# Kernel optimization log

Hardware: AMD Instinct MI355X
Metric: run time of the kernel (lower is better)

The kernel has to match this reference:

```python
import jax, jax.numpy as jnp
import numpy as np

N = 30000       # num atoms (all examples concatenated)
E = 480000      # total num edges (avg degree 16)
H = 128         # hidden_channels
R = 50          # num_rbf
NB = 3          # num interaction blocks
NEX = 64        # num examples (molecules)
NTYPES = 100    # atom type vocabulary
CUT = 10.0      # cutoff_upper


def setup_inputs() -> dict:
    key = jax.random.key(0)
    ks = jax.random.split(key, 20)
    s = 0.05
    inp = {
        "pos": jax.random.uniform(ks[0], (N, 3), dtype=jnp.float32) * 10.0,
        "atom_types": jax.random.randint(ks[1], (N,), 0, NTYPES),
        "edge_index": jax.random.randint(ks[2], (2, E), 0, N),
        "batch": jnp.sort(jax.random.randint(ks[3], (N,), 0, NEX)),
        # learned parameters
        "embedding": jax.random.normal(ks[4], (NTYPES, H), dtype=jnp.float32) * s,
        "filt_w1": jax.random.normal(ks[5], (NB, R, H), dtype=jnp.float32) * s,
        "filt_b1": jnp.zeros((NB, H), jnp.float32),
        "filt_w2": jax.random.normal(ks[6], (NB, H, H), dtype=jnp.float32) * s,
        "filt_b2": jnp.zeros((NB, H), jnp.float32),
        "lin1_w": jax.random.normal(ks[7], (NB, H, H), dtype=jnp.float32) * s,  # no bias
        "lin2_w": jax.random.normal(ks[8], (NB, H, H), dtype=jnp.float32) * s,
        "lin2_b": jnp.zeros((NB, H), jnp.float32),
        "blk_w": jax.random.normal(ks[9], (NB, H, H), dtype=jnp.float32) * s,
        "blk_b": jnp.zeros((NB, H), jnp.float32),
        "out_w1": jax.random.normal(ks[10], (H, H // 2), dtype=jnp.float32) * s,
        "out_b1": jnp.zeros((H // 2,), jnp.float32),
        "out_w2": jax.random.normal(ks[11], (H // 2, 1), dtype=jnp.float32) * s,
        "out_b2": jnp.zeros((1,), jnp.float32),
    }
    return inp


def reference(pos, atom_types, edge_index, batch, embedding,
              filt_w1, filt_b1, filt_w2, filt_b2,
              lin1_w, lin2_w, lin2_b, blk_w, blk_b,
              out_w1, out_b1, out_w2, out_b2):
    src, dst = edge_index[0], edge_index[1]
    # pairwise distances along edges
    diff = pos[src] - pos[dst]                        # [E,3]
    d = jnp.sqrt(jnp.sum(diff * diff, axis=-1) + 1e-12)  # [E]
    # Gaussian RBF expansion (PyG GaussianSmearing)
    offset = jnp.linspace(0.0, CUT, R, dtype=jnp.float32)
    coeff = -0.5 / (offset[1] - offset[0]) ** 2
    rbf = jnp.exp(coeff * (d[:, None] - offset) ** 2)  # [E,R]
    # cosine cutoff envelope
    C = 0.5 * (jnp.cos(d * jnp.pi / CUT) + 1.0) * (d < CUT)  # [E]

    x = embedding[atom_types]                         # [N,H]
    for b in range(NB):
        # filter network: Linear -> Tanh -> Linear, modulated by cutoff
        W = jnp.tanh(rbf @ filt_w1[b] + filt_b1[b]) @ filt_w2[b] + filt_b2[b]
        W = W * C[:, None]                            # [E,H]
        # cfconv: lin1 (no bias), gather-multiply-scatter, lin2
        h = x @ lin1_w[b]                             # [N,H]
        msg = h[src] * W                              # [E,H]
        agg = jax.ops.segment_sum(msg, dst, num_segments=N)  # [N,H]
        h = agg @ lin2_w[b] + lin2_b[b]
        # interaction block: activation + linear, residual update
        x = x + (jnp.tanh(h) @ blk_w[b] + blk_b[b])
    # output network: per-atom energy then scatter-sum per molecule
    e = jnp.tanh(x @ out_w1 + out_b1) @ out_w2 + out_b2     # [N,1]
    energy = jax.ops.segment_sum(e, batch, num_segments=NEX)  # [NEX,1]
    return energy.reshape(-1)
```

## Files before the change

kernel.cpp:

```cpp
#include <hip/hip_runtime.h>

typedef unsigned short ushort_t;
typedef _Float16 half8 __attribute__((ext_vector_type(8)));
typedef float f32x4 __attribute__((ext_vector_type(4)));

constexpr int NN  = 30000;
constexpr int EE  = 480000;
constexpr int NEXM = 64;
constexpr int ATB = 16;
constexpr int NSB = (NN + 255) / 256;
constexpr int NBINS = 2048;
constexpr int TROWS = 2064;

#define MFMA16(a,b,c) __builtin_amdgcn_mfma_f32_16x16x32_f16((a),(b),(c),0,0,0)
#define LDS_ADD(p,v) __hip_atomic_fetch_add((p),(v),__ATOMIC_RELAXED,__HIP_MEMORY_SCOPE_WORKGROUP)
#define LGKM_WAIT asm volatile("s_waitcnt lgkmcnt(0)" ::: "memory")

__device__ __forceinline__ float fast_tanh(float x){
  float e2 = __builtin_amdgcn_exp2f(x * 2.885390081777927f);
  return 1.f - 2.f * __builtin_amdgcn_rcpf(e2 + 1.f);
}
__device__ __forceinline__ ushort_t f2h(float v){
  union { _Float16 h; ushort_t s; } cv; cv.h = (_Float16)v; return cv.s;
}

__global__ __launch_bounds__(256) void prep_weights(
  const float* __restrict__ fw1, const float* __restrict__ fb1,
  const float* __restrict__ fw2, const float* __restrict__ l1w,
  const float* __restrict__ l2w, const float* __restrict__ bw,
  const float* __restrict__ ow1, ushort_t* __restrict__ frags)
{
  int u = blockIdx.x*256 + threadIdx.x;
  float val;
  if (u < 24576){
    int b = u >> 13; int v = u & 8191;
    int j = v & 7, lane = (v>>3)&63, fid = v>>9;
    int mt = fid>>1, ks = fid&1;
    int f1 = mt*16 + (lane&15);
    int k  = ks*32 + ((lane>>4)&3)*8 + j;
    val = (k < 50) ? fw1[(b*50 + k)*128 + f1] : (k == 50 ? fb1[b*128 + f1] : 0.f);
  } else if (u < 73728){
    int v = u - 24576; int b = v >> 14; int v2 = v & 16383;
    int j = v2&7, lane = (v2>>3)&63, fid = v2>>9;
    int mt = fid>>2, ks = fid&3;
    int n = mt*16 + (lane&15);
    int k = ks*32 + ((lane>>4)&3)*8 + j;
    val = fw2[b*16384 + k*128 + n];
  } else if (u < 221184){
    int v = u - 73728; int g = v / 49152; int v1 = v - g*49152;
    int b = v1 >> 14; int v2 = v1 & 16383;
    int j = v2&7, lane=(v2>>3)&63, fid=v2>>9;
    int mt = fid>>2, ks = fid&3;
    int n = mt*16 + (lane&15);
    int k = ks*32 + ((lane>>4)&3)*8 + j;
    const float* W = (g==0? l2w : (g==1? bw : l1w));
    val = W[b*16384 + k*128 + n];
  } else {
    int v2 = u - 221184;
    int j = v2&7, lane=(v2>>3)&63, fid=v2>>9;
    int mt = fid>>2, ks = fid&3;
    int n = mt*16 + (lane&15);
    int k = ks*32 + ((lane>>4)&3)*8 + j;
    val = ow1[k*64 + n];
  }
  frags[u] = f2h(val);
}

__global__ __launch_bounds__(256) void count_k(
  const int* __restrict__ ei, int* __restrict__ cnt)
{
  int e = blockIdx.x*256 + threadIdx.x;
  atomicAdd(cnt + ei[EE + e], 1);
}

__global__ __launch_bounds__(256) void scan1(
  const int* __restrict__ cnt, int* __restrict__ seg, int* __restrict__ bsum)
{
  __shared__ int ws[4];
  int i = blockIdx.x*256 + threadIdx.x;
  int lane = threadIdx.x & 63, w = threadIdx.x >> 6;
  int v = (i < NN) ? cnt[i] : 0;
  int s = v;
  #pragma unroll
  for (int o=1;o<64;o<<=1){ int t = __shfl_up(s,o,64); if (lane>=o) s += t; }
  if (lane == 63) ws[w] = s;
  __syncthreads();
  int add = 0;
  #pragma unroll
  for (int j=0;j<3;j++) if (w > j) add += ws[j];
  s += add;
  if (i < NN) seg[i] = s - v;
  if (threadIdx.x == 255) bsum[blockIdx.x] = s;
}

__global__ __launch_bounds__(128) void scan2(int* __restrict__ bsum)
{
  __shared__ int w0tot;
  int tid = threadIdx.x, lane = tid & 63, w = tid >> 6;
  int v = (tid < NSB) ? bsum[tid] : 0;
  int s = v;
  #pragma unroll
  for (int o=1;o<64;o<<=1){ int t = __shfl_up(s,o,64); if (lane>=o) s += t; }
  if (w == 0 && lane == 63) w0tot = s;
  __syncthreads();
  if (w == 1) s += w0tot;
  if (tid < NSB) bsum[tid] = s - v;
}

__global__ __launch_bounds__(256) void scan3(
  int* __restrict__ seg, const int* __restrict__ bsum)
{
  int i = blockIdx.x*256 + threadIdx.x;
  if (i < NN) seg[i] += bsum[blockIdx.x];
}

__global__ __launch_bounds__(256) void scatter_meta(
  const float* __restrict__ pos, const int* __restrict__ ei,
  int* __restrict__ off, uint2* __restrict__ meta2)
{
  int e = blockIdx.x*256 + threadIdx.x;
  int s = ei[e], d = ei[EE + e];
  float dx = pos[s*3+0]-pos[d*3+0];
  float dy = pos[s*3+1]-pos[d*3+1];
  float dz = pos[s*3+2]-pos[d*3+2];
  float dist = sqrtf(dx*dx+dy*dy+dz*dz + 1e-12f);
  float t = fminf(dist, 10.f) * ((float)NBINS / 10.f);
  int p = atomicAdd(off + d, 1);
  uint2 m;
  m.x = __float_as_uint(t);
  m.y = (unsigned)s;
  meta2[p] = m;
}

__global__ __launch_bounds__(256) void build_table(
  const ushort_t* __restrict__ w1a, const ushort_t* __restrict__ w2a,
  const float* __restrict__ fb2, ushort_t* __restrict__ tab)
{
  __shared__ ushort_t st[4*2112];
  const int wave = threadIdx.x>>6, lane = threadIdx.x&63;
  const int quad = lane>>4, n15 = lane&15;
  const int b = blockIdx.x / 33, tg = blockIdx.x % 33;
  const int tile = tg*4 + wave;
  if (tile >= TROWS/16) return;
  const half8* w1v = (const half8*)(w1a + b*8192);
  const half8* w2v = (const half8*)(w2a + b*16384);
  ushort_t* tw = st + wave*2112;
  half8 a1[16];
  #pragma unroll
  for (int i=0;i<16;i++) a1[i] = w1v[i*64 + lane];
  f32x4 b2v[8];
  #pragma unroll
  for (int mt=0;mt<8;mt++) b2v[mt] = *(const f32x4*)(fb2 + b*128 + mt*16 + quad*4);
  const f32x4 zero4 = {0.f,0.f,0.f,0.f};
  const float dd = 10.f/49.f;
  const float coefl2 = (-0.5f/(dd*dd)) * 1.4426950408889634f;
  const float dbin = 10.f/(float)NBINS;

  float de = (float)(tile*16 + n15) * dbin;
  float Cv = (de < 10.f) ? 0.5f*(cosf(de*0.31415926535897931f)+1.f) : 0.f;
  half8 rb0, rb1;
  #pragma unroll
  for (int j=0;j<8;j++){
    int k0 = quad*8 + j;
    float t0 = de - (float)k0*dd;
    rb0[j] = (_Float16)__builtin_amdgcn_exp2f(coefl2*t0*t0);
    int k1 = 32 + quad*8 + j;
    float v1;
    if (k1 < 50){ float t1 = de - (float)k1*dd; v1 = __builtin_amdgcn_exp2f(coefl2*t1*t1); }
    else v1 = (k1 == 50) ? 1.f : 0.f;
    rb1[j] = (_Float16)v1;
  }
  f32x4 acc1[8];
  #pragma unroll
  for (int mt=0;mt<8;mt++){
    acc1[mt] = MFMA16(a1[mt*2],   rb0, zero4);
    acc1[mt] = MFMA16(a1[mt*2+1], rb1, acc1[mt]);
  }
  #pragma unroll
  for (int mt=0;mt<8;mt++){
    union { ushort_t s[4]; uint2 v; } pk;
    #pragma unroll
    for (int r=0;r<4;r++) pk.s[r] = f2h(fast_tanh(acc1[mt][r]));
    *(uint2*)(tw + n15*132 + mt*16 + quad*4) = pk.v;
  }
  LGKM_WAIT;
  f32x4 acc2[8];
  #pragma unroll
  for (int mt=0;mt<8;mt++) acc2[mt] = zero4;
  #pragma unroll
  for (int ks=0;ks<4;ks++){
    const ushort_t* ra = tw + n15*132 + ks*32 + quad*8;
    union { uint2 v[2]; half8 h16; } cc;
    cc.v[0] = *(const uint2*)(ra);
    cc.v[1] = *(const uint2*)(ra + 4);
    half8 tb = cc.h16;
    #pragma unroll
    for (int mt=0;mt<8;mt++) acc2[mt] = MFMA16(w2v[(mt*4+ks)*64 + lane], tb, acc2[mt]);
  }
  LGKM_WAIT;
  #pragma unroll
  for (int mt=0;mt<8;mt++){
    f32x4 v = acc2[mt] + b2v[mt];
    union { ushort_t s[4]; uint2 q; } pk;
    #pragma unroll
    for (int r=0;r<4;r++) pk.s[r] = f2h(v[r] * Cv);
    *(uint2*)(tw + n15*132 + mt*16 + quad*4) = pk.q;
  }
  LGKM_WAIT;
  ushort_t* dstb = tab + ((size_t)b*TROWS + tile*16)*128;
  #pragma unroll
  for (int it=0;it<4;it++){
    int off = it*512 + lane*8;
    uint4 v = *(const uint4*)(tw + (off>>7)*132 + (off&127));
    *(uint4*)(dstb + (size_t)(off>>7)*128 + (off&127)) = v;
  }
}

__global__ __launch_bounds__(256) void embed_h0(
  const int* __restrict__ atype, const float* __restrict__ emb,
  const ushort_t* __restrict__ l1T, float* __restrict__ x, ushort_t* __restrict__ h)
{
  __shared__ float xbuf[4*2112];
  const int wave = threadIdx.x>>6, lane = threadIdx.x&63;
  const int quad = lane>>4, n15 = lane&15;
  float* xw = xbuf + wave*2112;
  ushort_t* sw = (ushort_t*)xw;
  const half8* wv = (const half8*)l1T;
  const f32x4 zero4 = {0.f,0.f,0.f,0.f};
  const int ntiles = NN/16;
  const int stride = gridDim.x*4;
  for (int tile = blockIdx.x*4 + wave; tile < ntiles; tile += stride){
    int a0 = tile*16;
    int typ = atype[a0 + n15];
    const f32x4* av = (const f32x4*)(emb + (size_t)typ*128);
    half8 bg[4]; f32x4 xl[4], xh[4];
    #pragma unroll
    for (int ks=0;ks<4;ks++){
      f32x4 lo = av[ks*8 + quad*2];
      f32x4 hi = av[ks*8 + quad*2 + 1];
      xl[ks] = lo; xh[ks] = hi;
      half8 bh;
      #pragma unroll
      for (int i=0;i<4;i++){ bh[i]=(_Float16)lo[i]; bh[4+i]=(_Float16)hi[i]; }
      bg[ks] = bh;
    }
    f32x4 acc[8];
    #pragma unroll
    for (int mt=0;mt<8;mt++) acc[mt] = zero4;
    #pragma unroll
    for (int ks=0;ks<4;ks++){
      #pragma unroll
      for (int mt=0;mt<8;mt++) acc[mt] = MFMA16(wv[(mt*4+ks)*64 + lane], bg[ks], acc[mt]);
    }
    #pragma unroll
    for (int ks=0;ks<4;ks++){
      *(f32x4*)(xw + n15*132 + ks*32 + quad*8)     = xl[ks];
      *(f32x4*)(xw + n15*132 + ks*32 + quad*8 + 4) = xh[ks];
    }
    LGKM_WAIT;
    {
      float* gx = x + (size_t)a0*128;
      #pragma unroll
      for (int it=0;it<8;it++){
        int off = it*256 + lane*4;
        f32x4 v = *(const f32x4*)(xw + (off>>7)*132 + (off&127));
        *(f32x4*)(gx + off) = v;
      }
    }
    LGKM_WAIT;
    #pragma unroll
    for (int mt=0;mt<8;mt++){
      union { ushort_t s[4]; uint2 v; } pk;
      #pragma unroll
      for (int r=0;r<4;r++) pk.s[r] = f2h(acc[mt][r]);
      *(uint2*)(sw + n15*132 + mt*16 + quad*4) = pk.v;
    }
    LGKM_WAIT;
    {
      ushort_t* gh = h + (size_t)a0*128;
      #pragma unroll
      for (int it=0;it<4;it++){
        int off = it*512 + lane*8;
        uint4 v = *(const uint4*)(sw + (off>>7)*132 + (off&127));
        *(uint4*)(gh + off) = v;
      }
    }
    LGKM_WAIT;
  }
}

__global__ __launch_bounds__(256,6) void mega_pass(
  const uint2* __restrict__ meta2, const ushort_t* __restrict__ hin,
  ushort_t* __restrict__ hout, const ushort_t* __restrict__ tab,
  const ushort_t* __restrict__ l2T, const ushort_t* __restrict__ bkT,
  const ushort_t* __restrict__ l1Tn,
  const float* __restrict__ l2b, const float* __restrict__ bb,
  const int* __restrict__ segend, float* __restrict__ x, int do_h)
{
  __shared__ ushort_t nt[2112];
  const int wave = threadIdx.x>>6, lane = threadIdx.x&63;
  const int quad = lane>>4, n15 = lane&15;
  const int base = blockIdx.x*ATB;
  const f32x4 zero4 = {0.f,0.f,0.f,0.f};

  const int cg = threadIdx.x >> 4, ctf = threadIdx.x & 15;
  const int ca = base + cg;
  const int clo = (ca==0) ? 0 : segend[ca-1];
  const int chi = segend[ca];
  float acc[8];
  #pragma unroll
  for (int j=0;j<8;j++) acc[j] = 0.f;

  if (clo < chi){
    uint2 me = *(const uint2*)(meta2 + clo);
    float t = __uint_as_float(me.x);
    int i0 = (int)t;
    float fr = t - (float)i0;
    const half8* tp = (const half8*)(tab + (size_t)i0*128) + ctf;
    half8 w0 = tp[0];
    half8 w1 = tp[16];
    half8 hv = *(const half8*)(hin + (size_t)me.y*128 + ctf*8);
    int e = clo;
    while (true){
      int en = e + 1;
      bool more = en < chi;
      half8 w0n = w0, w1n = w1, hvn = hv; float frn = fr;
      if (more){
        uint2 m2 = *(const uint2*)(meta2 + en);
        float t2 = __uint_as_float(m2.x);
        int i2 = (int)t2;
        frn = t2 - (float)i2;
        const half8* tpn = (const half8*)(tab + (size_t)i2*128) + ctf;
        w0n = tpn[0];
        w1n = tpn[16];
        hvn = *(const half8*)(hin + (size_t)m2.y*128 + ctf*8);
      }
      #pragma unroll
      for (int j=0;j<8;j++){
        float wl = (float)w0[j] + fr * ((float)w1[j] - (float)w0[j]);
        acc[j] += wl * (float)hv[j];
      }
      if (!more) break;
      w0 = w0n; w1 = w1n; hv = hvn; fr = frn; e = en;
    }
  }

  {
    union { ushort_t s[8]; uint4 q; } pk;
    #pragma unroll
    for (int j=0;j<8;j++) pk.s[j] = f2h(acc[j]);
    *(uint4*)(nt + cg*132 + ctf*8) = pk.q;
  }
  __syncthreads();

  {
    half8 bg[4];
    #pragma unroll
    for (int ks=0;ks<4;ks++){
      const ushort_t* ra = nt + n15*132 + ks*32 + quad*8;
      union { uint2 v[2]; half8 h16; } cc;
      cc.v[0] = *(const uint2*)(ra);
      cc.v[1] = *(const uint2*)(ra + 4);
      bg[ks] = cc.h16;
    }
    __syncthreads();
    const half8* wAv = (const half8*)l2T;
    f32x4 accA[2];
    #pragma unroll
    for (int i=0;i<2;i++) accA[i] = zero4;
    #pragma unroll
    for (int ks=0;ks<4;ks++){
      #pragma unroll
      for (int i=0;i<2;i++)
        accA[i] = MFMA16(wAv[((wave*2+i)*4+ks)*64 + lane], bg[ks], accA[i]);
    }
    #pragma unroll
    for (int i=0;i<2;i++){
      int mt = wave*2 + i;
      f32x4 bv = *(const f32x4*)(l2b + mt*16 + quad*4);
      union { ushort_t s[4]; uint2 v; } pk;
      #pragma unroll
      for (int r=0;r<4;r++) pk.s[r] = f2h(fast_tanh(accA[i][r] + bv[r]));
      *(uint2*)(nt + n15*132 + mt*16 + quad*4) = pk.v;
    }
    __syncthreads();
    half8 bg2[4];
    #pragma unroll
    for (int ks=0;ks<4;ks++){
      const ushort_t* ra = nt + n15*132 + ks*32 + quad*8;
      union { uint2 v[2]; half8 h16; } cc;
      cc.v[0] = *(const uint2*)(ra);
      cc.v[1] = *(const uint2*)(ra + 4);
      bg2[ks] = cc.h16;
    }
    __syncthreads();
    const half8* wBv = (const half8*)bkT;
    f32x4 accB[2];
    #pragma unroll
    for (int i=0;i<2;i++) accB[i] = zero4;
    #pragma unroll
    for (int ks=0;ks<4;ks++){
      #pragma unroll
      for (int i=0;i<2;i++)
        accB[i] = MFMA16(wBv[((wave*2+i)*4+ks)*64 + lane], bg2[ks], accB[i]);
    }
    f32x4 xn[2];
    float* xp = x + (size_t)(base + n15)*128;
    #pragma unroll
    for (int i=0;i<2;i++){
      int mt = wave*2 + i;
      f32x4 bv = *(const f32x4*)(bb + mt*16 + quad*4);
      f32x4 xv = *(const f32x4*)(xp + mt*16 + quad*4);
      xn[i] = xv + accB[i] + bv;
      *(f32x4*)(xp + mt*16 + quad*4) = xn[i];
    }
    if (do_h){
      #pragma unroll
      for (int i=0;i<2;i++){
        int mt = wave*2 + i;
        union { ushort_t s[4]; uint2 v; } pk;
        #pragma unroll
        for (int r=0;r<4;r++) pk.s[r] = f2h(xn[i][r]);
        *(uint2*)(nt + n15*132 + mt*16 + quad*4) = pk.v;
      }
      __syncthreads();
      half8 bg3[4];
      #pragma unroll
      for (int ks=0;ks<4;ks++){
        const ushort_t* ra = nt + n15*132 + ks*32 + quad*8;
        union { uint2 v[2]; half8 h16; } cc;
        cc.v[0] = *(const uint2*)(ra);
        cc.v[1] = *(const uint2*)(ra + 4);
        bg3[ks] = cc.h16;
      }
      const half8* wCv = (const half8*)l1Tn;
      f32x4 accC[2];
      #pragma unroll
      for (int i=0;i<2;i++) accC[i] = zero4;
      #pragma unroll
      for (int ks=0;ks<4;ks++){
        #pragma unroll
        for (int i=0;i<2;i++)
          accC[i] = MFMA16(wCv[((wave*2+i)*4+ks)*64 + lane], bg3[ks], accC[i]);
      }
      ushort_t* hp = hout + (size_t)(base + n15)*128;
      #pragma unroll
      for (int i=0;i<2;i++){
        int mt = wave*2 + i;
        union { ushort_t s[4]; uint2 v; } pk;
        #pragma unroll
        for (int r=0;r<4;r++) pk.s[r] = f2h(accC[i][r]);
        *(uint2*)(hp + mt*16 + quad*4) = pk.v;
      }
    }
  }
}

__global__ __launch_bounds__(256) void out_head(
  const float* __restrict__ x, const ushort_t* __restrict__ o1T,
  const float* __restrict__ ob1, const float* __restrict__ ow2,
  const float* __restrict__ ob2, const int* __restrict__ batch,
  float* __restrict__ out)
{
  __shared__ float part[NEXM];
  const int tid = threadIdx.x;
  if (tid < NEXM) part[tid] = 0.f;
  __syncthreads();
  const int wave = tid>>6, lane = tid&63;
  const int quad = lane>>4, n15 = lane&15;
  const half8* wv = (const half8*)o1T;
  const f32x4 zero4 = {0.f,0.f,0.f,0.f};
  f32x4 ow2v[4], ob1v[4];
  #pragma unroll
  for (int mt=0;mt<4;mt++){
    ow2v[mt] = *(const f32x4*)(ow2 + mt*16 + quad*4);
    ob1v[mt] = *(const f32x4*)(ob1 + mt*16 + quad*4);
  }
  const float ob2v = ob2[0];
  const int ntiles = NN/16;
  const int stride = gridDim.x*4;
  for (int tile = blockIdx.x*4 + wave; tile < ntiles; tile += stride){
    int a0 = tile*16;
    half8 bg[4];
    const f32x4* av = (const f32x4*)(x + (size_t)(a0 + n15)*128);
    #pragma unroll
    for (int ks=0;ks<4;ks++){
      f32x4 lo = av[ks*8 + quad*2];
      f32x4 hi = av[ks*8 + quad*2 + 1];
      half8 bh;
      #pragma unroll
      for (int i=0;i<4;i++){ bh[i]=(_Float16)lo[i]; bh[4+i]=(_Float16)hi[i]; }
      bg[ks] = bh;
    }
    f32x4 acc[4];
    #pragma unroll
    for (int mt=0;mt<4;mt++) acc[mt] = zero4;
    #pragma unroll
    for (int ks=0;ks<4;ks++){
      #pragma unroll
      for (int mt=0;mt<4;mt++) acc[mt] = MFMA16(wv[(mt*4+ks)*64 + lane], bg[ks], acc[mt]);
    }
    float e = 0.f;
    #pragma unroll
    for (int mt=0;mt<4;mt++){
      f32x4 v = acc[mt] + ob1v[mt];
      #pragma unroll
      for (int r=0;r<4;r++) e += fast_tanh(v[r]) * ow2v[mt][r];
    }
    e += __shfl_xor(e, 16, 64);
    e += __shfl_xor(e, 32, 64);
    if (quad == 0){
      int a = a0 + n15;
      LDS_ADD(&part[batch[a]], e + ob2v);
    }
  }
  __syncthreads();
  if (tid < NEXM)
    __hip_atomic_fetch_add(out + tid, part[tid], __ATOMIC_RELAXED, __HIP_MEMORY_SCOPE_AGENT);
}

extern "C" void kernel_launch(void* const* d_in, const int* in_sizes, int n_in,
                              void* d_out, int out_size, void* d_ws, size_t ws_size,
                              hipStream_t stream)
{
  const float* pos  = (const float*)d_in[0];
  const int*   atyp = (const int*)  d_in[1];
  const int*   ei   = (const int*)  d_in[2];
  const int*   bat  = (const int*)  d_in[3];
  const float* emb  = (const float*)d_in[4];
  const float* fw1  = (const float*)d_in[5];
  const float* fb1  = (const float*)d_in[6];
  const float* fw2  = (const float*)d_in[7];
  const float* fb2  = (const float*)d_in[8];
  const float* l1w  = (const float*)d_in[9];
  const float* l2w  = (const float*)d_in[10];
  const float* l2b  = (const float*)d_in[11];
  const float* bw   = (const float*)d_in[12];
  const float* bb   = (const float*)d_in[13];
  const float* ow1  = (const float*)d_in[14];
  const float* ob1  = (const float*)d_in[15];
  const float* ow2  = (const float*)d_in[16];
  const float* ob2  = (const float*)d_in[17];
  float* out = (float*)d_out;

  char* p = (char*)d_ws;
  uint2*    meta2 = (uint2*)p;   p += (size_t)EE*8;
  ushort_t* hA   = (ushort_t*)p; p += (size_t)NN*128*2;
  ushort_t* hB   = (ushort_t*)p; p += (size_t)NN*128*2;
  float*    x    = (float*)p;    p += (size_t)NN*128*4;
  ushort_t* frags = (ushort_t*)p; p += 229376*2;
  int*      segend = (int*)p;    p += (size_t)NN*4;
  int*      bsum  = (int*)p;     p += 512;
  ushort_t* tab  = (ushort_t*)p; p += (size_t)3*TROWS*128*2;

  int* cnt = (int*)x;

  ushort_t* w1T = frags;
  ushort_t* w2T = frags + 24576;
  ushort_t* l2T = frags + 73728;
  ushort_t* bkT = frags + 122880;
  ushort_t* l1T = frags + 172032;
  ushort_t* o1T = frags + 221184;

  hipMemsetAsync(d_out, 0, NEXM*sizeof(float), stream);
  hipMemsetAsync(cnt, 0, NN*sizeof(int), stream);
  prep_weights<<<896,256,0,stream>>>(fw1,fb1,fw2,l1w,l2w,bw,ow1,frags);
  build_table<<<99,256,0,stream>>>(w1T, w2T, fb2, tab);
  count_k<<<EE/256,256,0,stream>>>(ei, cnt);
  scan1<<<NSB,256,0,stream>>>(cnt, segend, bsum);
  scan2<<<1,128,0,stream>>>(bsum);
  scan3<<<NSB,256,0,stream>>>(segend, bsum);
  scatter_meta<<<EE/256,256,0,stream>>>(pos, ei, segend, meta2);
  embed_h0<<<512,256,0,stream>>>(atyp, emb, l1T, x, hA);

  for (int b=0;b<3;b++){
    const ushort_t* hin = (b & 1) ? hB : hA;
    ushort_t*       hoB = (b & 1) ? hA : hB;
    int do_h = (b < 2) ? 1 : 0;
    mega_pass<<<NN/ATB,256,0,stream>>>(meta2, hin, hoB,
                                       tab + (size_t)b*TROWS*128,
                                       l2T + b*16384, bkT + b*16384,
                                       l1T + ((b<2)?(b+1):0)*16384,
                                       l2b + b*128, bb + b*128,
                                       segend, x, do_h);
  }
  out_head<<<256,256,0,stream>>>(x, o1T, ob1, ow2, ob2, bat, out);
}
```

Before: 305.1 us.

## Interleave adjacent filter table rows and process two edges per loop iteration

```diff
diff --git a/kernel.cpp b/kernel.cpp
--- a/kernel.cpp
+++ b/kernel.cpp
@@ -134,7 +134,7 @@
 
 __global__ __launch_bounds__(256) void build_table(
   const ushort_t* __restrict__ w1a, const ushort_t* __restrict__ w2a,
-  const float* __restrict__ fb2, ushort_t* __restrict__ tab)
+  const float* __restrict__ fb2, ushort_t* __restrict__ tabP)
 {
   __shared__ ushort_t st[4*2112];
   const int wave = threadIdx.x>>6, lane = threadIdx.x&63;
@@ -207,12 +207,16 @@
     *(uint2*)(tw + n15*132 + mt*16 + quad*4) = pk.q;
   }
   LGKM_WAIT;
-  ushort_t* dstb = tab + ((size_t)b*TROWS + tile*16)*128;
+  ushort_t* dstb = tabP + (size_t)b*TROWS*256;
   #pragma unroll
   for (int it=0;it<4;it++){
     int off = it*512 + lane*8;
-    uint4 v = *(const uint4*)(tw + (off>>7)*132 + (off&127));
-    *(uint4*)(dstb + (size_t)(off>>7)*128 + (off&127)) = v;
+    int rl = off>>7, c = (off&127)>>3;
+    uint4 v = *(const uint4*)(tw + rl*132 + (off&127));
+    int R = tile*16 + rl;
+    *(uint4*)(dstb + (size_t)R*256 + c*16) = v;
+    if (R > 0)
+      *(uint4*)(dstb + (size_t)(R-1)*256 + c*16 + 8) = v;
   }
 }
 
@@ -291,7 +295,7 @@
 
 __global__ __launch_bounds__(256,6) void mega_pass(
   const uint2* __restrict__ meta2, const ushort_t* __restrict__ hin,
-  ushort_t* __restrict__ hout, const ushort_t* __restrict__ tab,
+  ushort_t* __restrict__ hout, const ushort_t* __restrict__ tabP,
   const ushort_t* __restrict__ l2T, const ushort_t* __restrict__ bkT,
   const ushort_t* __restrict__ l1Tn,
   const float* __restrict__ l2b, const float* __restrict__ bb,
@@ -312,36 +316,67 @@
   for (int j=0;j<8;j++) acc[j] = 0.f;
 
   if (clo < chi){
-    uint2 me = *(const uint2*)(meta2 + clo);
-    float t = __uint_as_float(me.x);
-    int i0 = (int)t;
-    float fr = t - (float)i0;
-    const half8* tp = (const half8*)(tab + (size_t)i0*128) + ctf;
-    half8 w0 = tp[0];
-    half8 w1 = tp[16];
-    half8 hv = *(const half8*)(hin + (size_t)me.y*128 + ctf*8);
+    const ushort_t* tbc  = tabP + ctf*16;
+    const ushort_t* hinc = hin + ctf*8;
+    uint2 m0 = meta2[clo];
+    uint2 m1 = (clo+1 < chi) ? meta2[clo+1] : m0;
+    float tA0 = __uint_as_float(m0.x);
+    int   iA0 = (int)tA0;  float fA0 = tA0 - (float)iA0;
+    const ushort_t* pA0 = tbc + (size_t)iA0*256;
+    half8 w0A0 = *(const half8*)pA0;
+    half8 w1A0 = *(const half8*)(pA0 + 8);
+    half8 hvA0 = *(const half8*)(hinc + (size_t)m0.y*128);
+    float tA1 = __uint_as_float(m1.x);
+    int   iA1 = (int)tA1;  float fA1 = tA1 - (float)iA1;
+    const ushort_t* pA1 = tbc + (size_t)iA1*256;
+    half8 w0A1 = *(const half8*)pA1;
+    half8 w1A1 = *(const half8*)(pA1 + 8);
+    half8 hvA1 = *(const half8*)(hinc + (size_t)m1.y*128);
     int e = clo;
-    while (true){
-      int en = e + 1;
-      bool more = en < chi;
-      half8 w0n = w0, w1n = w1, hvn = hv; float frn = fr;
-      if (more){
-        uint2 m2 = *(const uint2*)(meta2 + en);
-        float t2 = __uint_as_float(m2.x);
-        int i2 = (int)t2;
-        frn = t2 - (float)i2;
-        const half8* tpn = (const half8*)(tab + (size_t)i2*128) + ctf;
-        w0n = tpn[0];
-        w1n = tpn[16];
-        hvn = *(const half8*)(hin + (size_t)m2.y*128 + ctf*8);
+    uint2 n0, n1;
+    if (e+2 < chi){
+      n0 = meta2[e+2];
+      n1 = (e+3 < chi) ? meta2[e+3] : n0;
+    }
+    for (;;){
+      const bool hasNext = (e+2 < chi);
+      float fB0=fA0, fB1=fA1;
+      half8 w0B0=w0A0, w1B0=w1A0, hvB0=hvA0;
+      half8 w0B1=w0A1, w1B1=w1A1, hvB1=hvA1;
+      if (hasNext){
+        float tB0 = __uint_as_float(n0.x);
+        int iB0 = (int)tB0;  fB0 = tB0 - (float)iB0;
+        const ushort_t* pB0 = tbc + (size_t)iB0*256;
+        w0B0 = *(const half8*)pB0;
+        w1B0 = *(const half8*)(pB0 + 8);
+        hvB0 = *(const half8*)(hinc + (size_t)n0.y*128);
+        float tB1 = __uint_as_float(n1.x);
+        int iB1 = (int)tB1;  fB1 = tB1 - (float)iB1;
+        const ushort_t* pB1 = tbc + (size_t)iB1*256;
+        w0B1 = *(const half8*)pB1;
+        w1B1 = *(const half8*)(pB1 + 8);
+        hvB1 = *(const half8*)(hinc + (size_t)n1.y*128);
+        if (e+4 < chi){
+          n0 = meta2[e+4];
+          n1 = (e+5 < chi) ? meta2[e+5] : n0;
+        }
       }
       #pragma unroll
       for (int j=0;j<8;j++){
-        float wl = (float)w0[j] + fr * ((float)w1[j] - (float)w0[j]);
-        acc[j] += wl * (float)hv[j];
-      }
-      if (!more) break;
-      w0 = w0n; w1 = w1n; hv = hvn; fr = frn; e = en;
+        float wl = (float)w0A0[j] + fA0 * ((float)w1A0[j] - (float)w0A0[j]);
+        acc[j] += wl * (float)hvA0[j];
+      }
+      if (e+1 < chi){
+        #pragma unroll
+        for (int j=0;j<8;j++){
+          float wl = (float)w0A1[j] + fA1 * ((float)w1A1[j] - (float)w0A1[j]);
+          acc[j] += wl * (float)hvA1[j];
+        }
+      }
+      if (!hasNext) break;
+      fA0=fB0; w0A0=w0B0; w1A0=w1B0; hvA0=hvB0;
+      fA1=fB1; w0A1=w0B1; w1A1=w1B1; hvA1=hvB1;
+      e += 2;
     }
   }
 
@@ -551,7 +586,7 @@
   ushort_t* frags = (ushort_t*)p; p += 229376*2;
   int*      segend = (int*)p;    p += (size_t)NN*4;
   int*      bsum  = (int*)p;     p += 512;
-  ushort_t* tab  = (ushort_t*)p; p += (size_t)3*TROWS*128*2;
+  ushort_t* tabP = (ushort_t*)p; p += (size_t)3*TROWS*256*2;
 
   int* cnt = (int*)x;
 
@@ -565,7 +600,7 @@
   hipMemsetAsync(d_out, 0, NEXM*sizeof(float), stream);
   hipMemsetAsync(cnt, 0, NN*sizeof(int), stream);
   prep_weights<<<896,256,0,stream>>>(fw1,fb1,fw2,l1w,l2w,bw,ow1,frags);
-  build_table<<<99,256,0,stream>>>(w1T, w2T, fb2, tab);
+  build_table<<<99,256,0,stream>>>(w1T, w2T, fb2, tabP);
   count_k<<<EE/256,256,0,stream>>>(ei, cnt);
   scan1<<<NSB,256,0,stream>>>(cnt, segend, bsum);
   scan2<<<1,128,0,stream>>>(bsum);
@@ -578,7 +613,7 @@
     ushort_t*       hoB = (b & 1) ? hA : hB;
     int do_h = (b < 2) ? 1 : 0;
     mega_pass<<<NN/ATB,256,0,stream>>>(meta2, hin, hoB,
-                                       tab + (size_t)b*TROWS*128,
+                                       tabP + (size_t)b*TROWS*256,
                                        l2T + b*16384, bkT + b*16384,
                                        l1T + ((b<2)?(b+1):0)*16384,
                                        l2b + b*128, bb + b*128,
```

After: 335.3 us. 1.1x slower.

## Split each atom's edge aggregation across four lane groups with shuffle reduction

Applied to the files above, without the earlier changes.

```diff
diff --git a/kernel.cpp b/kernel.cpp
--- a/kernel.cpp
+++ b/kernel.cpp
@@ -207,7 +207,7 @@
     *(uint2*)(tw + n15*132 + mt*16 + quad*4) = pk.q;
   }
   LGKM_WAIT;
-  ushort_t* dstb = tab + ((size_t)b*TROWS + tile*16)*128;
+  ushort_t* dstb = tab + ((size_t)tile*16)*128 + (size_t)b*TROWS*128;
   #pragma unroll
   for (int it=0;it<4;it++){
     int off = it*512 + lane*8;
@@ -302,54 +302,70 @@
   const int quad = lane>>4, n15 = lane&15;
   const int base = blockIdx.x*ATB;
   const f32x4 zero4 = {0.f,0.f,0.f,0.f};
-
-  const int cg = threadIdx.x >> 4, ctf = threadIdx.x & 15;
-  const int ca = base + cg;
-  const int clo = (ca==0) ? 0 : segend[ca-1];
-  const int chi = segend[ca];
-  float acc[8];
-  #pragma unroll
-  for (int j=0;j<8;j++) acc[j] = 0.f;
-
-  if (clo < chi){
-    uint2 me = *(const uint2*)(meta2 + clo);
-    float t = __uint_as_float(me.x);
-    int i0 = (int)t;
-    float fr = t - (float)i0;
-    const half8* tp = (const half8*)(tab + (size_t)i0*128) + ctf;
-    half8 w0 = tp[0];
-    half8 w1 = tp[16];
-    half8 hv = *(const half8*)(hin + (size_t)me.y*128 + ctf*8);
-    int e = clo;
-    while (true){
-      int en = e + 1;
-      bool more = en < chi;
-      half8 w0n = w0, w1n = w1, hvn = hv; float frn = fr;
-      if (more){
-        uint2 m2 = *(const uint2*)(meta2 + en);
-        float t2 = __uint_as_float(m2.x);
-        int i2 = (int)t2;
-        frn = t2 - (float)i2;
-        const half8* tpn = (const half8*)(tab + (size_t)i2*128) + ctf;
-        w0n = tpn[0];
-        w1n = tpn[16];
-        hvn = *(const half8*)(hin + (size_t)m2.y*128 + ctf*8);
+  const int sub = lane>>4, ctf = lane&15;
+
+  #pragma unroll 1
+  for (int q=0; q<4; ++q){
+    const int cg = wave*4 + q;
+    const int ca = base + cg;
+    const int clo = (ca==0) ? 0 : segend[ca-1];
+    const int chi = segend[ca];
+    float acc[8];
+    #pragma unroll
+    for (int j=0;j<8;j++) acc[j] = 0.f;
+
+    if (clo < chi){
+      const int elast = chi - 1;
+      int e0 = clo + sub;
+      uint2 mcur = meta2[(e0 < chi) ? e0 : elast];
+      int e1 = clo + 4 + sub;
+      uint2 mnxt = meta2[(e1 < chi) ? e1 : elast];
+      float t0 = __uint_as_float(mcur.x);
+      int i0 = (int)t0; float fr = t0 - (float)i0;
+      const half8* tp = (const half8*)(tab + (size_t)i0*128) + ctf;
+      half8 w0 = tp[0];
+      half8 w1 = tp[16];
+      half8 hv = *(const half8*)(hin + (size_t)mcur.y*128 + ctf*8);
+      bool val = (e0 < chi);
+
+      for (int eb = clo; ; ){
+        int ebn = eb + 4;
+        bool more = ebn < chi;
+        half8 w0n=w0, w1n=w1, hvn=hv; float frn=fr; bool valn=val;
+        if (more){
+          float tn = __uint_as_float(mnxt.x);
+          int in_ = (int)tn; frn = tn - (float)in_;
+          const half8* tpn = (const half8*)(tab + (size_t)in_*128) + ctf;
+          w0n = tpn[0];
+          w1n = tpn[16];
+          hvn = *(const half8*)(hin + (size_t)mnxt.y*128 + ctf*8);
+          valn = (ebn + sub < chi);
+          int e2 = ebn + 4 + sub;
+          mnxt = meta2[(e2 < chi) ? e2 : elast];
+        }
+        if (val){
+          #pragma unroll
+          for (int j=0;j<8;j++){
+            float wl = (float)w0[j] + fr * ((float)w1[j] - (float)w0[j]);
+            acc[j] += wl * (float)hv[j];
+          }
+        }
+        if (!more) break;
+        w0=w0n; w1=w1n; hv=hvn; fr=frn; val=valn; eb=ebn;
       }
-      #pragma unroll
-      for (int j=0;j<8;j++){
-        float wl = (float)w0[j] + fr * ((float)w1[j] - (float)w0[j]);
-        acc[j] += wl * (float)hv[j];
-      }
-      if (!more) break;
-      w0 = w0n; w1 = w1n; hv = hvn; fr = frn; e = en;
-    }
-  }
-
-  {
-    union { ushort_t s[8]; uint4 q; } pk;
-    #pragma unroll
-    for (int j=0;j<8;j++) pk.s[j] = f2h(acc[j]);
-    *(uint4*)(nt + cg*132 + ctf*8) = pk.q;
+    }
+
+    #pragma unroll
+    for (int j=0;j<8;j++){
+      acc[j] += __shfl_xor(acc[j], 16, 64);
+      acc[j] += __shfl_xor(acc[j], 32, 64);
+    }
+    if (sub == 0){
+      union { ushort_t s[8]; uint4 qv; } pk;
+      #pragma unroll
+      for (int j=0;j<8;j++) pk.s[j] = f2h(acc[j]);
+      *(uint4*)(nt + cg*132 + ctf*8) = pk.qv;
+    }
   }
   __syncthreads();
 
```

New measurement: 307.9 us. About the same (+0.9%).

## Pack edge metadata, pair table rows, balance edge gather per wave, fuse output head

Applied to the files above, without the earlier changes.

```diff
diff --git a/kernel.cpp b/kernel.cpp
--- a/kernel.cpp
+++ b/kernel.cpp
@@ -116,7 +116,7 @@
 
 __global__ __launch_bounds__(256) void scatter_meta(
   const float* __restrict__ pos, const int* __restrict__ ei,
-  int* __restrict__ off, uint2* __restrict__ meta2)
+  int* __restrict__ off, unsigned* __restrict__ meta1)
 {
   int e = blockIdx.x*256 + threadIdx.x;
   int s = ei[e], d = ei[EE + e];
@@ -125,11 +125,10 @@
   float dz = pos[s*3+2]-pos[d*3+2];
   float dist = sqrtf(dx*dx+dy*dy+dz*dz + 1e-12f);
   float t = fminf(dist, 10.f) * ((float)NBINS / 10.f);
+  int bin = (int)t;
+  int frq = (int)((t - (float)bin) * 16.f);
   int p = atomicAdd(off + d, 1);
-  uint2 m;
-  m.x = __float_as_uint(t);
-  m.y = (unsigned)s;
-  meta2[p] = m;
+  meta1[p] = ((unsigned)s << 16) | ((unsigned)frq << 12) | (unsigned)bin;
 }
 
 __global__ __launch_bounds__(256) void build_table(
@@ -207,13 +206,29 @@
     *(uint2*)(tw + n15*132 + mt*16 + quad*4) = pk.q;
   }
   LGKM_WAIT;
-  ushort_t* dstb = tab + ((size_t)b*TROWS + tile*16)*128;
+  ushort_t* dstb = tab + ((size_t)tile*16)*128 + (size_t)b*TROWS*128;
   #pragma unroll
   for (int it=0;it<4;it++){
     int off = it*512 + lane*8;
     uint4 v = *(const uint4*)(tw + (off>>7)*132 + (off&127));
     *(uint4*)(dstb + (size_t)(off>>7)*128 + (off&127)) = v;
   }
+}
+
+__global__ __launch_bounds__(256) void pair_table(
+  const ushort_t* __restrict__ tab, ushort_t* __restrict__ tabP)
+{
+  int u = blockIdx.x*256 + threadIdx.x;
+  if (u >= 3*2063*16) return;
+  int b = u / (2063*16); int v = u - b*(2063*16);
+  int i = v >> 4, c = v & 15;
+  const ushort_t* rb = tab + (size_t)b*TROWS*128;
+  half8 r0 = *(const half8*)(rb + (size_t)i*128 + c*8);
+  half8 r1 = *(const half8*)(rb + (size_t)(i+1)*128 + c*8);
+  half8 dl = r1 - r0;
+  ushort_t* dst = tabP + (size_t)b*TROWS*256 + (size_t)i*256 + c*16;
+  *(half8*)dst = r0;
+  *(half8*)(dst+8) = dl;
 }
 
 __global__ __launch_bounds__(256) void embed_h0(
@@ -290,66 +305,106 @@
 }
 
 __global__ __launch_bounds__(256,6) void mega_pass(
-  const uint2* __restrict__ meta2, const ushort_t* __restrict__ hin,
-  ushort_t* __restrict__ hout, const ushort_t* __restrict__ tab,
+  const unsigned* __restrict__ meta1, const ushort_t* __restrict__ hin,
+  ushort_t* __restrict__ hout, const ushort_t* __restrict__ tabP,
   const ushort_t* __restrict__ l2T, const ushort_t* __restrict__ bkT,
-  const ushort_t* __restrict__ l1Tn,
+  const ushort_t* __restrict__ l1Tn, const ushort_t* __restrict__ o1T,
   const float* __restrict__ l2b, const float* __restrict__ bb,
-  const int* __restrict__ segend, float* __restrict__ x, int do_h)
-{
+  const float* __restrict__ ob1, const float* __restrict__ ow2,
+  const float* __restrict__ ob2, const int* __restrict__ batch,
+  float* __restrict__ out,
+  const int* __restrict__ segend, float* __restrict__ x, int do_h, int last)
+{
+  __shared__ float ntf[16*132];
   __shared__ ushort_t nt[2112];
   const int wave = threadIdx.x>>6, lane = threadIdx.x&63;
   const int quad = lane>>4, n15 = lane&15;
   const int base = blockIdx.x*ATB;
   const f32x4 zero4 = {0.f,0.f,0.f,0.f};
-
-  const int cg = threadIdx.x >> 4, ctf = threadIdx.x & 15;
-  const int ca = base + cg;
-  const int clo = (ca==0) ? 0 : segend[ca-1];
-  const int chi = segend[ca];
+  const int sub = lane>>4, ctf = lane&15;
+
+  for (int z=threadIdx.x; z<16*132; z+=256) ntf[z] = 0.f;
+  __syncthreads();
+
+  const int a0 = base + wave*4;
+  const int wlo = (a0==0) ? 0 : segend[a0-1];
+  const int whi = segend[a0+3];
+  const int b0 = segend[a0], b1 = segend[a0+1], b2 = segend[a0+2];
   float acc[8];
   #pragma unroll
   for (int j=0;j<8;j++) acc[j] = 0.f;
-
-  if (clo < chi){
-    uint2 me = *(const uint2*)(meta2 + clo);
-    float t = __uint_as_float(me.x);
-    int i0 = (int)t;
-    float fr = t - (float)i0;
-    const half8* tp = (const half8*)(tab + (size_t)i0*128) + ctf;
-    half8 w0 = tp[0];
-    half8 w1 = tp[16];
-    half8 hv = *(const half8*)(hin + (size_t)me.y*128 + ctf*8);
-    int e = clo;
-    while (true){
-      int en = e + 1;
-      bool more = en < chi;
-      half8 w0n = w0, w1n = w1, hvn = hv; float frn = fr;
-      if (more){
-        uint2 m2 = *(const uint2*)(meta2 + en);
-        float t2 = __uint_as_float(m2.x);
-        int i2 = (int)t2;
-        frn = t2 - (float)i2;
-        const half8* tpn = (const half8*)(tab + (size_t)i2*128) + ctf;
-        w0n = tpn[0];
-        w1n = tpn[16];
-        hvn = *(const half8*)(hin + (size_t)m2.y*128 + ctf*8);
-      }
-      #pragma unroll
-      for (int j=0;j<8;j++){
-        float wl = (float)w0[j] + fr * ((float)w1[j] - (float)w0[j]);
-        acc[j] += wl * (float)hv[j];
-      }
-      if (!more) break;
-      w0 = w0n; w1 = w1n; hv = hvn; fr = frn; e = en;
-    }
-  }
+  int cur = -1;
+
+  const int nst = (whi - wlo + 3) >> 2;
+  if (nst > 0){
+    float frA, frB, frC;
+    half8 w0A, dlA, hvA, w0B, dlB, hvB, w0C, dlC, hvC;
+    int drA, drB, drC;
+    bool vaA, vaB, vaC;
+
+#define ISSUE(S, EB) { \
+  int e_ = (EB) + sub; \
+  bool v_ = e_ < whi; \
+  int ec_ = v_ ? e_ : (whi-1); \
+  unsigned m_ = meta1[ec_]; \
+  int bin_ = (int)(m_ & 4095u); \
+  fr##S = ((float)((m_>>12)&15u) + 0.5f) * 0.0625f; \
+  const ushort_t* tp_ = tabP + (size_t)bin_*256 + ctf*16; \
+  w0##S = *(const half8*)tp_; \
+  dl##S = *(const half8*)(tp_ + 8); \
+  hv##S = *(const half8*)(hin + (size_t)(m_>>16)*128 + ctf*8); \
+  va##S = v_; \
+  dr##S = (e_>=b0) + (e_>=b1) + (e_>=b2); \
+}
+#define CONSUME(S) { \
+  if (va##S){ \
+    if (dr##S != cur){ \
+      if (cur >= 0){ \
+        float* np_ = ntf + (wave*4 + cur)*132 + ctf*8; \
+        _Pragma("unroll") \
+        for (int j_=0;j_<8;j_++){ LDS_ADD(np_+j_, acc[j_]); acc[j_] = 0.f; } \
+      } \
+      cur = dr##S; \
+    } \
+    _Pragma("unroll") \
+    for (int j_=0;j_<8;j_++){ \
+      float wl_ = (float)w0##S[j_] + fr##S * (float)dl##S[j_]; \
+      acc[j_] += wl_ * (float)hv##S[j_]; \
+    } \
+  } \
+}
+    ISSUE(A, wlo)
+    if (nst > 1) ISSUE(B, wlo+4)
+    if (nst > 2) ISSUE(C, wlo+8)
+    int i = 0;
+    for (;;){
+      CONSUME(A)
+      if (++i == nst) break;
+      if (i + 2 < nst) ISSUE(A, wlo + 4*(i+2))
+      CONSUME(B)
+      if (++i == nst) break;
+      if (i + 2 < nst) ISSUE(B, wlo + 4*(i+2))
+      CONSUME(C)
+      if (++i == nst) break;
+      if (i + 2 < nst) ISSUE(C, wlo + 4*(i+2))
+    }
+    if (cur >= 0){
+      float* np_ = ntf + (wave*4 + cur)*132 + ctf*8;
+      #pragma unroll
+      for (int j_=0;j_<8;j_++) LDS_ADD(np_+j_, acc[j_]);
+    }
+#undef ISSUE
+#undef CONSUME
+  }
+  __syncthreads();
 
   {
+    int cg = threadIdx.x>>4, c = threadIdx.x&15;
+    const float* np = ntf + cg*132 + c*8;
     union { ushort_t s[8]; uint4 q; } pk;
     #pragma unroll
-    for (int j=0;j<8;j++) pk.s[j] = f2h(acc[j]);
-    *(uint4*)(nt + cg*132 + ctf*8) = pk.q;
+    for (int j=0;j<8;j++) pk.s[j] = f2h(np[j]);
+    *(uint4*)(nt + cg*132 + c*8) = pk.q;
   }
   __syncthreads();
 
@@ -412,7 +467,7 @@
       f32x4 bv = *(const f32x4*)(bb + mt*16 + quad*4);
       f32x4 xv = *(const f32x4*)(xp + mt*16 + quad*4);
       xn[i] = xv + accB[i] + bv;
-      *(f32x4*)(xp + mt*16 + quad*4) = xn[i];
+      if (!last) *(f32x4*)(xp + mt*16 + quad*4) = xn[i];
     }
     if (do_h){
       #pragma unroll
@@ -452,71 +507,54 @@
         for (int r=0;r<4;r++) pk.s[r] = f2h(accC[i][r]);
         *(uint2*)(hp + mt*16 + quad*4) = pk.v;
       }
-    }
-  }
-}
-
-__global__ __launch_bounds__(256) void out_head(
-  const float* __restrict__ x, const ushort_t* __restrict__ o1T,
-  const float* __restrict__ ob1, const float* __restrict__ ow2,
-  const float* __restrict__ ob2, const int* __restrict__ batch,
-  float* __restrict__ out)
-{
-  __shared__ float part[NEXM];
-  const int tid = threadIdx.x;
-  if (tid < NEXM) part[tid] = 0.f;
-  __syncthreads();
-  const int wave = tid>>6, lane = tid&63;
-  const int quad = lane>>4, n15 = lane&15;
-  const half8* wv = (const half8*)o1T;
-  const f32x4 zero4 = {0.f,0.f,0.f,0.f};
-  f32x4 ow2v[4], ob1v[4];
-  #pragma unroll
-  for (int mt=0;mt<4;mt++){
-    ow2v[mt] = *(const f32x4*)(ow2 + mt*16 + quad*4);
-    ob1v[mt] = *(const f32x4*)(ob1 + mt*16 + quad*4);
-  }
-  const float ob2v = ob2[0];
-  const int ntiles = NN/16;
-  const int stride = gridDim.x*4;
-  for (int tile = blockIdx.x*4 + wave; tile < ntiles; tile += stride){
-    int a0 = tile*16;
-    half8 bg[4];
-    const f32x4* av = (const f32x4*)(x + (size_t)(a0 + n15)*128);
-    #pragma unroll
-    for (int ks=0;ks<4;ks++){
-      f32x4 lo = av[ks*8 + quad*2];
-      f32x4 hi = av[ks*8 + quad*2 + 1];
-      half8 bh;
-      #pragma unroll
-      for (int i=0;i<4;i++){ bh[i]=(_Float16)lo[i]; bh[4+i]=(_Float16)hi[i]; }
-      bg[ks] = bh;
-    }
-    f32x4 acc[4];
-    #pragma unroll
-    for (int mt=0;mt<4;mt++) acc[mt] = zero4;
-    #pragma unroll
-    for (int ks=0;ks<4;ks++){
-      #pragma unroll
-      for (int mt=0;mt<4;mt++) acc[mt] = MFMA16(wv[(mt*4+ks)*64 + lane], bg[ks], acc[mt]);
-    }
-    float e = 0.f;
-    #pragma unroll
-    for (int mt=0;mt<4;mt++){
-      f32x4 v = acc[mt] + ob1v[mt];
-      #pragma unroll
-      for (int r=0;r<4;r++) e += fast_tanh(v[r]) * ow2v[mt][r];
-    }
-    e += __shfl_xor(e, 16, 64);
-    e += __shfl_xor(e, 32, 64);
-    if (quad == 0){
-      int a = a0 + n15;
-      LDS_ADD(&part[batch[a]], e + ob2v);
-    }
-  }
-  __syncthreads();
-  if (tid < NEXM)
-    __hip_atomic_fetch_add(out + tid, part[tid], __ATOMIC_RELAXED, __HIP_MEMORY_SCOPE_AGENT);
+    } else if (last){
+      #pragma unroll
+      for (int i=0;i<2;i++){
+        int mt = wave*2 + i;
+        union { ushort_t s[4]; uint2 v; } pk;
+        #pragma unroll
+        for (int r=0;r<4;r++) pk.s[r] = f2h(xn[i][r]);
+        *(uint2*)(nt + n15*132 + mt*16 + quad*4) = pk.v;
+      }
+      __syncthreads();
+      if (wave == 0){
+        half8 bg3[4];
+        #pragma unroll
+        for (int ks=0;ks<4;ks++){
+          const ushort_t* ra = nt + n15*132 + ks*32 + quad*8;
+          union { uint2 v[2]; half8 h16; } cc;
+          cc.v[0] = *(const uint2*)(ra);
+          cc.v[1] = *(const uint2*)(ra + 4);
+          bg3[ks] = cc.h16;
+        }
+        const half8* wv = (const half8*)o1T;
+        f32x4 acco[4];
+        #pragma unroll
+        for (int mt=0;mt<4;mt++) acco[mt] = zero4;
+        #pragma unroll
+        for (int ks=0;ks<4;ks++){
+          #pragma unroll
+          for (int mt=0;mt<4;mt++) acco[mt] = MFMA16(wv[(mt*4+ks)*64 + lane], bg3[ks], acco[mt]);
+        }
+        float e = 0.f;
+        #pragma unroll
+        for (int mt=0;mt<4;mt++){
+          f32x4 bv = *(const f32x4*)(ob1 + mt*16 + quad*4);
+          f32x4 wo = *(const f32x4*)(ow2 + mt*16 + quad*4);
+          f32x4 v = acco[mt] + bv;
+          #pragma unroll
+          for (int r=0;r<4;r++) e += fast_tanh(v[r]) * wo[r];
+        }
+        e += __shfl_xor(e, 16, 64);
+        e += __shfl_xor(e, 32, 64);
+        if (quad == 0){
+          int a = base + n15;
+          __hip_atomic_fetch_add(out + batch[a], e + ob2[0],
+                                 __ATOMIC_RELAXED, __HIP_MEMORY_SCOPE_AGENT);
+        }
+      }
+    }
+  }
 }
 
 extern "C" void kernel_launch(void* const* d_in, const int* in_sizes, int n_in,
@@ -544,7 +582,7 @@
   float* out = (float*)d_out;
 
   char* p = (char*)d_ws;
-  uint2*    meta2 = (uint2*)p;   p += (size_t)EE*8;
+  unsigned* meta1 = (unsigned*)p; p += (size_t)EE*4;
   ushort_t* hA   = (ushort_t*)p; p += (size_t)NN*128*2;
   ushort_t* hB   = (ushort_t*)p; p += (size_t)NN*128*2;
   float*    x    = (float*)p;    p += (size_t)NN*128*4;
@@ -552,6 +590,7 @@
   int*      segend = (int*)p;    p += (size_t)NN*4;
   int*      bsum  = (int*)p;     p += 512;
   ushort_t* tab  = (ushort_t*)p; p += (size_t)3*TROWS*128*2;
+  ushort_t* tabP = (ushort_t*)p; p += (size_t)3*TROWS*256*2;
 
   int* cnt = (int*)x;
 
@@ -566,23 +605,25 @@
   hipMemsetAsync(cnt, 0, NN*sizeof(int), stream);
   prep_weights<<<896,256,0,stream>>>(fw1,fb1,fw2,l1w,l2w,bw,ow1,frags);
   build_table<<<99,256,0,stream>>>(w1T, w2T, fb2, tab);
+  pair_table<<<387,256,0,stream>>>(tab, tabP);
   count_k<<<EE/256,256,0,stream>>>(ei, cnt);
   scan1<<<NSB,256,0,stream>>>(cnt, segend, bsum);
   scan2<<<1,128,0,stream>>>(bsum);
   scan3<<<NSB,256,0,stream>>>(segend, bsum);
-  scatter_meta<<<EE/256,256,0,stream>>>(pos, ei, segend, meta2);
+  scatter_meta<<<EE/256,256,0,stream>>>(pos, ei, segend, meta1);
   embed_h0<<<512,256,0,stream>>>(atyp, emb, l1T, x, hA);
 
   for (int b=0;b<3;b++){
     const ushort_t* hin = (b & 1) ? hB : hA;
     ushort_t*       hoB = (b & 1) ? hA : hB;
     int do_h = (b < 2) ? 1 : 0;
-    mega_pass<<<NN/ATB,256,0,stream>>>(meta2, hin, hoB,
-                                       tab + (size_t)b*TROWS*128,
+    int last = (b == 2) ? 1 : 0;
+    mega_pass<<<NN/ATB,256,0,stream>>>(meta1, hin, hoB,
+                                       tabP + (size_t)b*TROWS*256,
                                        l2T + b*16384, bkT + b*16384,
-                                       l1T + ((b<2)?(b+1):0)*16384,
+                                       l1T + ((b<2)?(b+1):0)*16384, o1T,
                                        l2b + b*128, bb + b*128,
-                                       segend, x, do_h);
-  }
-  out_head<<<256,256,0,stream>>>(x, o1T, ob1, ow2, ob2, bat, out);
-}
+                                       ob1, ow2, ob2, bat, out,
+                                       segend, x, do_h, last);
+  }
+}
```

Measured after the change: 681.6 us. 123% more time.
